# Optimization experiments

Hardware: AMD Instinct MI355X
Metric: run time of the kernel (lower is better)

The kernel has to match this reference:

```python
import jax, jax.numpy as jnp
import numpy as np

N_USERS, N_ITEMS = 100000, 100000
N_NODES = N_USERS + N_ITEMS
N_EDGES = 4000000
USER_DIM, ITEM_DIM = 256, 128
COMMON, HIDDEN, OUT = 64, 64, 32


def setup_inputs() -> dict:
    key = jax.random.key(0)
    ks = jax.random.split(key, 12)
    inp = {
        "user_tensor": jax.random.normal(ks[0], (N_USERS, USER_DIM), jnp.float32),
        "item_tensor": jax.random.normal(ks[1], (N_ITEMS, ITEM_DIM), jnp.float32),
        "edge_index": jax.random.randint(ks[2], (2, N_EDGES), 0, N_NODES, jnp.int64),
        "edge_weight": jax.random.uniform(ks[3], (N_EDGES,), jnp.float32),
        # user_proj / item_proj (nn.Linear: y = x @ W + b)
        "Wu": jax.random.normal(ks[4], (USER_DIM, COMMON), jnp.float32) / np.sqrt(USER_DIM),
        "bu": jnp.zeros((COMMON,), jnp.float32),
        "Wi": jax.random.normal(ks[5], (ITEM_DIM, COMMON), jnp.float32) / np.sqrt(ITEM_DIM),
        "bi": jnp.zeros((COMMON,), jnp.float32),
        # GCNConv layers (linear without bias + separate bias)
        "W1": jax.random.normal(ks[6], (COMMON, HIDDEN), jnp.float32) / np.sqrt(COMMON),
        "b1": jnp.zeros((HIDDEN,), jnp.float32),
        "W2": jax.random.normal(ks[7], (HIDDEN, OUT), jnp.float32) / np.sqrt(HIDDEN),
        "b2": jnp.zeros((OUT,), jnp.float32),
    }
    return inp


def gcn_conv(x, W, b, src, dst, ew, num_nodes):
    """PyG GCNConv: add self-loops (weight 1), symmetric deg norm, transform, scatter-add."""
    x = x @ W  # transform first: [N, out]
    loop = jnp.arange(num_nodes, dtype=src.dtype)
    src2 = jnp.concatenate([src, loop])
    dst2 = jnp.concatenate([dst, loop])
    ew2 = jnp.concatenate([ew, jnp.ones((num_nodes,), x.dtype)])
    deg = jax.ops.segment_sum(ew2, dst2, num_segments=num_nodes)
    dinv = jnp.where(deg > 0, jax.lax.rsqrt(deg), 0.0)
    norm = dinv[src2] * ew2 * dinv[dst2]  # [E+N]
    msgs = x[src2] * norm[:, None]  # gather + scale: [E+N, out]
    return jax.ops.segment_sum(msgs, dst2, num_segments=num_nodes) + b


def reference(user_tensor, item_tensor, edge_index, edge_weight,
              Wu, bu, Wi, bi, W1, b1, W2, b2):
    user_emb = user_tensor @ Wu + bu
    item_emb = item_tensor @ Wi + bi
    x = jnp.concatenate([user_emb, item_emb], axis=0)  # [N_NODES, COMMON]
    src, dst = edge_index[0], edge_index[1]
    x = gcn_conv(x, W1, b1, src, dst, edge_weight, N_NODES)
    x = jax.nn.relu(x)
    x = gcn_conv(x, W2, b2, src, dst, edge_weight, N_NODES)
    return x
```

## Files before the change

kernel.cpp:

```cpp
#include <hip/hip_runtime.h>
#include <hip/hip_bf16.h>

#define N_USERS_C 100000
#define N_ITEMS_C 100000
#define N_NODES_C 200000
#define USER_DIM_C 256
#define ITEM_DIM_C 128
#define COMMON_C 64
#define HIDDEN_C 64
#define OUT_DIM_C 32

#define CB_BITS 8
#define CB_NODES 256
#define NCB ((N_NODES_C + CB_NODES - 1) / CB_NODES)
#define CB_CAP 5632
#define B_THREADS 256
#define B_UNROLL (CB_CAP / B_THREADS)

#define BIN_GRID 512
#define BIN_CHUNK_MAX 8192
#define MAX_EPT 8

#define UBLK 1563

typedef unsigned int uint32;
typedef __bf16 bf16x8 __attribute__((ext_vector_type(8)));
typedef float f32x4 __attribute__((ext_vector_type(4)));



__device__ __forceinline__ float bf2f(ushort u) { return __uint_as_float(((unsigned)u) << 16); }
__device__ __forceinline__ ushort f2bf(float f) {
    unsigned u = __float_as_uint(f);
    return (ushort)((u + 0x7FFFu + ((u >> 16) & 1u)) >> 16);
}
__device__ __forceinline__ void store4(float* p, float a, float b, float c, float d) {
    *(float4*)p = make_float4(a, b, c, d);
}
__device__ __forceinline__ void store4(ushort* p, float a, float b, float c, float d) {
    ushort4 u;
    u.x = f2bf(a); u.y = f2bf(b); u.z = f2bf(c); u.w = f2bf(d);
    *(ushort4*)p = u;
}

union ABFrag {
    uint4 q;
    ushort u[8];
    bf16x8 v;
};


__device__ __forceinline__ void wt_one(const float* W, ushort* WT, int K, int N, int i) {
    int k = i / N, n = i % N;
    WT[(size_t)n * K + k] = f2bf(W[i]);
}


__global__ __launch_bounds__(1024) void bin_kernel(
        const int* __restrict__ src, const int* __restrict__ dst,
        const float* __restrict__ ew, int* __restrict__ bucket_cnt,
        uint2* __restrict__ rec2, int E, int chunk,
        const float* __restrict__ Wu, const float* __restrict__ Wi,
        const float* __restrict__ W1, const float* __restrict__ W2,
        ushort* __restrict__ wtU, ushort* __restrict__ wtI,
        ushort* __restrict__ wt1, ushort* __restrict__ wt2) {
    {
        const int SU = USER_DIM_C * 64, SI = ITEM_DIM_C * 64, S1 = 64 * 64, S2 = 64 * 32;
        int i = blockIdx.x * 1024 + threadIdx.x;
        if (i < SU + SI + S1 + S2) {
            if (i < SU) wt_one(Wu, wtU, USER_DIM_C, 64, i);
            else if ((i -= SU) < SI) wt_one(Wi, wtI, ITEM_DIM_C, 64, i);
            else if ((i -= SI) < S1) wt_one(W1, wt1, 64, 64, i);
            else wt_one(W2, wt2, 64, 32, i - S1);
        }
    }

    __shared__ int hist[NCB];
    __shared__ int cur[NCB];
    for (int i = threadIdx.x; i < NCB; i += 1024) hist[i] = 0;
    __syncthreads();
    const int beg = blockIdx.x * chunk;
    const int end = min(E, beg + chunk);

    int dc[MAX_EPT];
#pragma unroll
    for (int s = 0; s < MAX_EPT / 4; ++s) {
        const int e0 = beg + (threadIdx.x << 2) + (s << 12);
        int4 d4 = make_int4(-1, -1, -1, -1);
        if (e0 + 3 < end) {
            d4 = *(const int4*)(dst + e0);
        } else if (e0 < end) {
            d4.x = dst[e0];
            if (e0 + 1 < end) d4.y = dst[e0 + 1];
            if (e0 + 2 < end) d4.z = dst[e0 + 2];
        }
        dc[s * 4 + 0] = d4.x; dc[s * 4 + 1] = d4.y;
        dc[s * 4 + 2] = d4.z; dc[s * 4 + 3] = d4.w;
        if (d4.x >= 0) atomicAdd(&hist[d4.x >> CB_BITS], 1);
        if (d4.y >= 0) atomicAdd(&hist[d4.y >> CB_BITS], 1);
        if (d4.z >= 0) atomicAdd(&hist[d4.z >> CB_BITS], 1);
        if (d4.w >= 0) atomicAdd(&hist[d4.w >> CB_BITS], 1);
    }
    __syncthreads();

    for (int i = threadIdx.x; i < NCB; i += 1024) {
        const int h = hist[i];
        cur[i] = h ? atomicAdd(&bucket_cnt[i], h) : 0;
    }
    __syncthreads();

#pragma unroll
    for (int s = 0; s < MAX_EPT / 4; ++s) {
        const int e0 = beg + (threadIdx.x << 2) + (s << 12);
        if (e0 >= end) continue;
        int4 s4;
        float4 w4;
        if (e0 + 3 < end) {
            s4 = *(const int4*)(src + e0);
            w4 = *(const float4*)(ew + e0);
        } else {
            s4 = make_int4(0, 0, 0, 0);
            w4 = make_float4(0, 0, 0, 0);
            s4.x = src[e0]; w4.x = ew[e0];
            if (e0 + 1 < end) { s4.y = src[e0 + 1]; w4.y = ew[e0 + 1]; }
            if (e0 + 2 < end) { s4.z = src[e0 + 2]; w4.z = ew[e0 + 2]; }
        }
        const int dv[4] = {dc[s * 4 + 0], dc[s * 4 + 1], dc[s * 4 + 2], dc[s * 4 + 3]};
        const int sv[4] = {s4.x, s4.y, s4.z, s4.w};
        const float wv[4] = {w4.x, w4.y, w4.z, w4.w};
#pragma unroll
        for (int k = 0; k < 4; ++k) {
            const int d = dv[k];
            if (d < 0) continue;
            uint32 q = (uint32)(wv[k] * 255.0f + 0.5f);
            if (q > 255u) q = 255u;
            const int b = d >> CB_BITS;
            const int slot = atomicAdd(&cur[b], 1);
            if (slot < CB_CAP)
                rec2[(size_t)b * CB_CAP + slot] =
                    make_uint2((((uint32)sv[k]) << 8) | q, (uint32)d);
        }
    }
}


__global__ __launch_bounds__(B_THREADS) void region_build_kernel(
        const uint2* __restrict__ rec2, const int* __restrict__ bucket_cnt,
        uint32* __restrict__ csr32, int* __restrict__ row_beg,
        int* __restrict__ row_cnt, float* __restrict__ dinv) {
    __shared__ int pk[CB_NODES];
    __shared__ int s[CB_NODES];
    __shared__ int cur[CB_NODES];
    const int cb = blockIdx.x;
    const int node0 = cb << CB_BITS;
    int total = bucket_cnt[cb];
    if (total > CB_CAP) total = CB_CAP;
    const uint2* r = rec2 + (size_t)cb * CB_CAP;

    pk[threadIdx.x] = 0;
    __syncthreads();

    uint2 rr[B_UNROLL];
#pragma unroll
    for (int u = 0; u < B_UNROLL; ++u) {
        const int j = threadIdx.x + u * B_THREADS;
        if (j < total) {
            rr[u] = r[j];
            atomicAdd(&pk[rr[u].y & (CB_NODES - 1)],
                      (int)((1u << 20) | (rr[u].x & 255u)));
        } else {
            rr[u] = make_uint2(0u, 0xFFFFFFFFu);
        }
    }
    __syncthreads();

    const int v = pk[threadIdx.x] >> 20;
    s[threadIdx.x] = v;
    __syncthreads();
#pragma unroll
    for (int off = 1; off < CB_NODES; off <<= 1) {
        const int t = (threadIdx.x >= off) ? s[threadIdx.x - off] : 0;
        __syncthreads();
        s[threadIdx.x] += t;
        __syncthreads();
    }
    {
        const int ex = s[threadIdx.x] - v;
        const int node = node0 + threadIdx.x;
        const int abs0 = cb * (2 * CB_CAP) + ex;
        if (node < N_NODES_C) {
            row_beg[node] = abs0;
            row_cnt[node] = v;
            dinv[node] = rsqrtf(1.0f + (float)(pk[threadIdx.x] & 0xFFFFF) * (1.0f / 255.0f));
        }
        cur[threadIdx.x] = abs0;
    }
    __syncthreads();

#pragma unroll
    for (int u = 0; u < B_UNROLL; ++u) {
        if (rr[u].y != 0xFFFFFFFFu) {
            const int slot = atomicAdd(&cur[rr[u].y & (CB_NODES - 1)], 1);
            csr32[slot] = rr[u].x;
        }
    }
}


template <int K>
__global__ __launch_bounds__(256) void fused_proj_kernel(
        const float* __restrict__ X, const ushort* __restrict__ WT,
        const ushort* __restrict__ wt1, const float* __restrict__ bias,
        const float* __restrict__ dinv, ushort* __restrict__ y1, int node0) {
    __shared__ ushort elds[64][72];
    const int lane = threadIdx.x & 63;
    const int wave = threadIdx.x >> 6;
    const int lr = lane & 15;
    const int quad = lane >> 4;

    const int M = N_USERS_C;
    const int m0 = blockIdx.x * 64 + wave * 16;

    f32x4 acc[4];
#pragma unroll
    for (int nt = 0; nt < 4; ++nt) acc[nt] = (f32x4){0.0f, 0.0f, 0.0f, 0.0f};

    int arow = m0 + lr;
    if (arow >= M) arow = M - 1;
    const float* Xr = X + (size_t)arow * K;

#pragma unroll
    for (int kc = 0; kc < K; kc += 32) {
        const int k0 = kc + quad * 8;
        float4 x0 = *(const float4*)(Xr + k0);
        float4 x1 = *(const float4*)(Xr + k0 + 4);
        ABFrag a;
        a.u[0] = f2bf(x0.x); a.u[1] = f2bf(x0.y); a.u[2] = f2bf(x0.z); a.u[3] = f2bf(x0.w);
        a.u[4] = f2bf(x1.x); a.u[5] = f2bf(x1.y); a.u[6] = f2bf(x1.z); a.u[7] = f2bf(x1.w);
#pragma unroll
        for (int nt = 0; nt < 4; ++nt) {
            ABFrag bf;
            bf.q = *(const uint4*)(WT + (size_t)(nt * 16 + lr) * K + k0);
            acc[nt] = __builtin_amdgcn_mfma_f32_16x16x32_bf16(a.v, bf.v, acc[nt], 0, 0, 0);
        }
    }

#pragma unroll
    for (int r = 0; r < 4; ++r) {
        const int row_l = wave * 16 + quad * 4 + r;
#pragma unroll
        for (int nt = 0; nt < 4; ++nt) {
            const int n = nt * 16 + lr;
            elds[row_l][n] = f2bf(acc[nt][r] + bias[n]);
        }
    }
    __syncthreads();

    f32x4 acc2[4];
#pragma unroll
    for (int nt = 0; nt < 4; ++nt) acc2[nt] = (f32x4){0.0f, 0.0f, 0.0f, 0.0f};

#pragma unroll
    for (int kc = 0; kc < 64; kc += 32) {
        const int k0 = kc + quad * 8;
        ABFrag a;
        a.q = *(const uint4*)(&elds[wave * 16 + lr][k0]);
#pragma unroll
        for (int nt = 0; nt < 4; ++nt) {
            ABFrag bf;
            bf.q = *(const uint4*)(wt1 + (size_t)(nt * 16 + lr) * 64 + k0);
            acc2[nt] = __builtin_amdgcn_mfma_f32_16x16x32_bf16(a.v, bf.v, acc2[nt], 0, 0, 0);
        }
    }

#pragma unroll
    for (int r = 0; r < 4; ++r) {
        const int m = m0 + quad * 4 + r;
        if (m < M) {
            const int node = node0 + m;
            const float sc = dinv[node];
#pragma unroll
            for (int nt = 0; nt < 4; ++nt) {
                y1[(size_t)node * 64 + nt * 16 + lr] = f2bf(acc2[nt][r] * sc);
            }
        }
    }
}

template <int K, int NT, bool XF32, bool SCALE>
__global__ __launch_bounds__(256) void mfma_proj_kernel(const void* __restrict__ Xv,
                                                        const ushort* __restrict__ WT,
                                                        const float* __restrict__ bias,
                                                        const float* __restrict__ dinvp,
                                                        ushort* __restrict__ Y, int M) {
    const int lane = threadIdx.x & 63;
    const int wave = threadIdx.x >> 6;
    const int lr = lane & 15;
    const int quad = lane >> 4;
    const int m0 = blockIdx.x * 64 + wave * 16;
    const int N = NT * 16;

    f32x4 acc[NT];
#pragma unroll
    for (int nt = 0; nt < NT; ++nt) acc[nt] = (f32x4){0.0f, 0.0f, 0.0f, 0.0f};

    int arow = m0 + lr;
    if (arow >= M) arow = M - 1;
    const size_t abase = (size_t)arow * K;

#pragma unroll
    for (int kc = 0; kc < K; kc += 32) {
        const int k0 = kc + quad * 8;
        ABFrag a;
        if (XF32) {
            const float* Xf = (const float*)Xv;
            float4 x0 = *(const float4*)(Xf + abase + k0);
            float4 x1 = *(const float4*)(Xf + abase + k0 + 4);
            a.u[0] = f2bf(x0.x); a.u[1] = f2bf(x0.y); a.u[2] = f2bf(x0.z); a.u[3] = f2bf(x0.w);
            a.u[4] = f2bf(x1.x); a.u[5] = f2bf(x1.y); a.u[6] = f2bf(x1.z); a.u[7] = f2bf(x1.w);
        } else {
            const ushort* Xb = (const ushort*)Xv;
            a.q = *(const uint4*)(Xb + abase + k0);
        }
#pragma unroll
        for (int nt = 0; nt < NT; ++nt) {
            ABFrag bf;
            bf.q = *(const uint4*)(WT + (size_t)(nt * 16 + lr) * K + k0);
            acc[nt] = __builtin_amdgcn_mfma_f32_16x16x32_bf16(a.v, bf.v, acc[nt], 0, 0, 0);
        }
    }

#pragma unroll
    for (int r = 0; r < 4; ++r) {
        const int m = m0 + quad * 4 + r;
        if (m < M) {
            const float sc = SCALE ? dinvp[m] : 1.0f;
#pragma unroll
            for (int nt = 0; nt < NT; ++nt) {
                const int n = nt * 16 + lr;
                const float bc = bias ? bias[n] : 0.0f;
                Y[(size_t)m * N + n] = f2bf((acc[nt][r] + bc) * sc);
            }
        }
    }
}


template <int N, bool RELU, typename TY>
__global__ void gather_kernel(const int* __restrict__ row_beg, const int* __restrict__ row_cnt,
                              const uint32* __restrict__ csr, const ushort* __restrict__ y,
                              const float* __restrict__ dinv, const float* __restrict__ b,
                              TY* __restrict__ out) {
    constexpr int LPN = N / 4;
    const int node = blockIdx.x * (256 / LPN) + threadIdx.x / LPN;
    const int c0 = (threadIdx.x % LPN) * 4;

    const int beg = row_beg[node];
    const int end = beg + row_cnt[node];

    float a0[4] = {0, 0, 0, 0}, a1[4] = {0, 0, 0, 0}, a2[4] = {0, 0, 0, 0}, a3[4] = {0, 0, 0, 0};
    int j = beg;
    for (; j + 4 <= end; j += 4) {
        uint32 e0 = csr[j], e1 = csr[j + 1], e2 = csr[j + 2], e3 = csr[j + 3];
        int s0 = e0 >> 8, s1 = e1 >> 8, s2 = e2 >> 8, s3 = e3 >> 8;
        float c0v = (float)(e0 & 255u) * (1.0f / 255.0f);
        float c1v = (float)(e1 & 255u) * (1.0f / 255.0f);
        float c2v = (float)(e2 & 255u) * (1.0f / 255.0f);
        float c3v = (float)(e3 & 255u) * (1.0f / 255.0f);
        ushort4 u0 = *(const ushort4*)(y + (size_t)s0 * N + c0);
        ushort4 u1 = *(const ushort4*)(y + (size_t)s1 * N + c0);
        ushort4 u2 = *(const ushort4*)(y + (size_t)s2 * N + c0);
        ushort4 u3 = *(const ushort4*)(y + (size_t)s3 * N + c0);
        a0[0] += bf2f(u0.x) * c0v; a0[1] += bf2f(u0.y) * c0v;
        a0[2] += bf2f(u0.z) * c0v; a0[3] += bf2f(u0.w) * c0v;
        a1[0] += bf2f(u1.x) * c1v; a1[1] += bf2f(u1.y) * c1v;
        a1[2] += bf2f(u1.z) * c1v; a1[3] += bf2f(u1.w) * c1v;
        a2[0] += bf2f(u2.x) * c2v; a2[1] += bf2f(u2.y) * c2v;
        a2[2] += bf2f(u2.z) * c2v; a2[3] += bf2f(u2.w) * c2v;
        a3[0] += bf2f(u3.x) * c3v; a3[1] += bf2f(u3.y) * c3v;
        a3[2] += bf2f(u3.z) * c3v; a3[3] += bf2f(u3.w) * c3v;
    }
    for (; j < end; ++j) {
        uint32 e = csr[j];
        int s = e >> 8;
        float cv = (float)(e & 255u) * (1.0f / 255.0f);
        ushort4 u = *(const ushort4*)(y + (size_t)s * N + c0);
        a0[0] += bf2f(u.x) * cv; a0[1] += bf2f(u.y) * cv;
        a0[2] += bf2f(u.z) * cv; a0[3] += bf2f(u.w) * cv;
    }
    const float di = dinv[node];
    ushort4 us = *(const ushort4*)(y + (size_t)node * N + c0);
    float4 bc = *(const float4*)(b + c0);
    float r0 = (((a0[0] + a1[0]) + (a2[0] + a3[0])) + bf2f(us.x)) * di + bc.x;
    float r1 = (((a0[1] + a1[1]) + (a2[1] + a3[1])) + bf2f(us.y)) * di + bc.y;
    float r2 = (((a0[2] + a1[2]) + (a2[2] + a3[2])) + bf2f(us.z)) * di + bc.z;
    float r3 = (((a0[3] + a1[3]) + (a2[3] + a3[3])) + bf2f(us.w)) * di + bc.w;
    if (RELU) {
        r0 = fmaxf(r0, 0.0f); r1 = fmaxf(r1, 0.0f);
        r2 = fmaxf(r2, 0.0f); r3 = fmaxf(r3, 0.0f);
    }
    store4(&out[(size_t)node * N + c0], r0, r1, r2, r3);
}


extern "C" void kernel_launch(void* const* d_in, const int* in_sizes, int n_in,
                              void* d_out, int out_size, void* d_ws, size_t ws_size,
                              hipStream_t stream) {
    const float* user = (const float*)d_in[0];
    const float* item = (const float*)d_in[1];
    const int* ei = (const int*)d_in[2];
    const float* ew = (const float*)d_in[3];
    const float* Wu = (const float*)d_in[4];
    const float* bu = (const float*)d_in[5];
    const float* Wi = (const float*)d_in[6];
    const float* bi = (const float*)d_in[7];
    const float* W1 = (const float*)d_in[8];
    const float* b1 = (const float*)d_in[9];
    const float* W2 = (const float*)d_in[10];
    const float* b2 = (const float*)d_in[11];
    float* out = (float*)d_out;

    const int E = in_sizes[3];
    const int* src = ei;
    const int* dst = ei + E;
    const int NB = N_NODES_C;
    const int nblk = (E > BIN_GRID * BIN_CHUNK_MAX) ? ((E + BIN_CHUNK_MAX - 1) / BIN_CHUNK_MAX)
                                                    : BIN_GRID;
    const int chunk = (((E + nblk - 1) / nblk) + 3) & ~3;

    char* p = (char*)d_ws;
    uint2* rec2 = (uint2*)p;   p += (size_t)NCB * CB_CAP * 8;
    ushort* y1 = (ushort*)p;   p += (size_t)NB * 64 * 2;
    ushort* h1 = (ushort*)p;   p += (size_t)NB * 64 * 2;
    ushort* y2 = (ushort*)p;   p += (size_t)NB * 32 * 2;
    int* bucket_cnt = (int*)p; p += (size_t)NCB * 4;
    int* row_beg = (int*)p;    p += (size_t)NB * 4;
    int* row_cnt = (int*)p;    p += (size_t)NB * 4;
    float* dinv = (float*)p;   p += (size_t)NB * 4;
    ushort* wtU = (ushort*)p;  p += (size_t)USER_DIM_C * 64 * 2;
    ushort* wtI = (ushort*)p;  p += (size_t)ITEM_DIM_C * 64 * 2;
    ushort* wt1 = (ushort*)p;  p += (size_t)64 * 64 * 2;
    ushort* wt2 = (ushort*)p;  p += (size_t)64 * 32 * 2;

    uint32* csr = (uint32*)rec2;

    hipMemsetAsync(bucket_cnt, 0, (size_t)NCB * 4, stream);
    bin_kernel<<<nblk, 1024, 0, stream>>>(src, dst, ew, bucket_cnt, rec2, E, chunk,
                                          Wu, Wi, W1, W2, wtU, wtI, wt1, wt2);
    region_build_kernel<<<NCB, B_THREADS, 0, stream>>>(rec2, bucket_cnt, csr, row_beg, row_cnt,
                                                       dinv);

    fused_proj_kernel<USER_DIM_C><<<UBLK, 256, 0, stream>>>(user, wtU, wt1, bu, dinv, y1, 0);
    fused_proj_kernel<ITEM_DIM_C><<<UBLK, 256, 0, stream>>>(item, wtI, wt1, bi, dinv, y1,
                                                            N_USERS_C);

    gather_kernel<64, true><<<NB / 16, 256, 0, stream>>>(row_beg, row_cnt, csr, y1, dinv, b1, h1);

    mfma_proj_kernel<64, 2, false, true><<<NB / 64, 256, 0, stream>>>(
        h1, wt2, (const float*)nullptr, dinv, y2, NB);
    gather_kernel<32, false><<<NB / 32, 256, 0, stream>>>(row_beg, row_cnt, csr, y2, dinv, b2, out);
}
```

Measured before the change: 509.8 us.

## Fuse layer-1 gather with layer-2 projection and merge user/item projection launches

Merges the user and item projection kernels into one launch that dispatches by block index, and hoists all input loads ahead of the MFMA loop so more memory requests are in flight. Fuses the first GCN aggregation (with bias and ReLU) with the second linear transform: each block stages 16 aggregated rows in shared memory and one wave runs the 64x32 MFMA, so the h1 intermediate is never written to or read back from global memory. This removes one kernel launch and a full intermediate round trip. In exchange, only one wave per block does the MFMA step and the hoisted loads raise register use.

```diff
diff --git a/kernel.cpp b/kernel.cpp
--- a/kernel.cpp
+++ b/kernel.cpp
@@ -36,11 +36,6 @@
 }
 __device__ __forceinline__ void store4(float* p, float a, float b, float c, float d) {
     *(float4*)p = make_float4(a, b, c, d);
-}
-__device__ __forceinline__ void store4(ushort* p, float a, float b, float c, float d) {
-    ushort4 u;
-    u.x = f2bf(a); u.y = f2bf(b); u.z = f2bf(c); u.w = f2bf(d);
-    *(ushort4*)p = u;
 }
 
 union ABFrag {
@@ -208,40 +203,51 @@
 
 
 template <int K>
-__global__ __launch_bounds__(256) void fused_proj_kernel(
+__device__ __forceinline__ void fused_proj_body(
         const float* __restrict__ X, const ushort* __restrict__ WT,
         const ushort* __restrict__ wt1, const float* __restrict__ bias,
-        const float* __restrict__ dinv, ushort* __restrict__ y1, int node0) {
-    __shared__ ushort elds[64][72];
+        const float* __restrict__ dinv, ushort* __restrict__ y1, int node0, int mb,
+        ushort (*elds)[72]) {
+    constexpr int NK = K / 32;
     const int lane = threadIdx.x & 63;
     const int wave = threadIdx.x >> 6;
     const int lr = lane & 15;
     const int quad = lane >> 4;
 
     const int M = N_USERS_C;
-    const int m0 = blockIdx.x * 64 + wave * 16;
-
-    f32x4 acc[4];
-#pragma unroll
-    for (int nt = 0; nt < 4; ++nt) acc[nt] = (f32x4){0.0f, 0.0f, 0.0f, 0.0f};
+    const int m0 = mb * 64 + wave * 16;
 
     int arow = m0 + lr;
     if (arow >= M) arow = M - 1;
-    const float* Xr = X + (size_t)arow * K;
-
-#pragma unroll
-    for (int kc = 0; kc < K; kc += 32) {
-        const int k0 = kc + quad * 8;
-        float4 x0 = *(const float4*)(Xr + k0);
-        float4 x1 = *(const float4*)(Xr + k0 + 4);
-        ABFrag a;
-        a.u[0] = f2bf(x0.x); a.u[1] = f2bf(x0.y); a.u[2] = f2bf(x0.z); a.u[3] = f2bf(x0.w);
-        a.u[4] = f2bf(x1.x); a.u[5] = f2bf(x1.y); a.u[6] = f2bf(x1.z); a.u[7] = f2bf(x1.w);
+    const float* Xr = X + (size_t)arow * K + quad * 8;
+
+    float4 xf[2 * NK];
+#pragma unroll
+    for (int t = 0; t < NK; ++t) {
+        xf[2 * t] = *(const float4*)(Xr + t * 32);
+        xf[2 * t + 1] = *(const float4*)(Xr + t * 32 + 4);
+    }
+    ABFrag xa[NK];
+#pragma unroll
+    for (int t = 0; t < NK; ++t) {
+        xa[t].u[0] = f2bf(xf[2 * t].x); xa[t].u[1] = f2bf(xf[2 * t].y);
+        xa[t].u[2] = f2bf(xf[2 * t].z); xa[t].u[3] = f2bf(xf[2 * t].w);
+        xa[t].u[4] = f2bf(xf[2 * t + 1].x); xa[t].u[5] = f2bf(xf[2 * t + 1].y);
+        xa[t].u[6] = f2bf(xf[2 * t + 1].z); xa[t].u[7] = f2bf(xf[2 * t + 1].w);
+    }
+
+    f32x4 acc[4];
+#pragma unroll
+    for (int nt = 0; nt < 4; ++nt) acc[nt] = (f32x4){0.0f, 0.0f, 0.0f, 0.0f};
+
+#pragma unroll
+    for (int t = 0; t < NK; ++t) {
+        const int k0 = t * 32 + quad * 8;
 #pragma unroll
         for (int nt = 0; nt < 4; ++nt) {
             ABFrag bf;
             bf.q = *(const uint4*)(WT + (size_t)(nt * 16 + lr) * K + k0);
-            acc[nt] = __builtin_amdgcn_mfma_f32_16x16x32_bf16(a.v, bf.v, acc[nt], 0, 0, 0);
+            acc[nt] = __builtin_amdgcn_mfma_f32_16x16x32_bf16(xa[t].v, bf.v, acc[nt], 0, 0, 0);
         }
     }
 
@@ -287,59 +293,104 @@
     }
 }
 
-template <int K, int NT, bool XF32, bool SCALE>
-__global__ __launch_bounds__(256) void mfma_proj_kernel(const void* __restrict__ Xv,
-                                                        const ushort* __restrict__ WT,
-                                                        const float* __restrict__ bias,
-                                                        const float* __restrict__ dinvp,
-                                                        ushort* __restrict__ Y, int M) {
-    const int lane = threadIdx.x & 63;
-    const int wave = threadIdx.x >> 6;
-    const int lr = lane & 15;
-    const int quad = lane >> 4;
-    const int m0 = blockIdx.x * 64 + wave * 16;
-    const int N = NT * 16;
-
-    f32x4 acc[NT];
-#pragma unroll
-    for (int nt = 0; nt < NT; ++nt) acc[nt] = (f32x4){0.0f, 0.0f, 0.0f, 0.0f};
-
-    int arow = m0 + lr;
-    if (arow >= M) arow = M - 1;
-    const size_t abase = (size_t)arow * K;
-
-#pragma unroll
-    for (int kc = 0; kc < K; kc += 32) {
-        const int k0 = kc + quad * 8;
-        ABFrag a;
-        if (XF32) {
-            const float* Xf = (const float*)Xv;
-            float4 x0 = *(const float4*)(Xf + abase + k0);
-            float4 x1 = *(const float4*)(Xf + abase + k0 + 4);
-            a.u[0] = f2bf(x0.x); a.u[1] = f2bf(x0.y); a.u[2] = f2bf(x0.z); a.u[3] = f2bf(x0.w);
-            a.u[4] = f2bf(x1.x); a.u[5] = f2bf(x1.y); a.u[6] = f2bf(x1.z); a.u[7] = f2bf(x1.w);
-        } else {
-            const ushort* Xb = (const ushort*)Xv;
-            a.q = *(const uint4*)(Xb + abase + k0);
-        }
-#pragma unroll
-        for (int nt = 0; nt < NT; ++nt) {
-            ABFrag bf;
-            bf.q = *(const uint4*)(WT + (size_t)(nt * 16 + lr) * K + k0);
-            acc[nt] = __builtin_amdgcn_mfma_f32_16x16x32_bf16(a.v, bf.v, acc[nt], 0, 0, 0);
-        }
-    }
-
-#pragma unroll
-    for (int r = 0; r < 4; ++r) {
-        const int m = m0 + quad * 4 + r;
-        if (m < M) {
-            const float sc = SCALE ? dinvp[m] : 1.0f;
-#pragma unroll
-            for (int nt = 0; nt < NT; ++nt) {
-                const int n = nt * 16 + lr;
-                const float bc = bias ? bias[n] : 0.0f;
-                Y[(size_t)m * N + n] = f2bf((acc[nt][r] + bc) * sc);
+__global__ __launch_bounds__(256) void fused_proj_kernel(
+        const float* __restrict__ user, const float* __restrict__ item,
+        const ushort* __restrict__ wtU, const ushort* __restrict__ wtI,
+        const ushort* __restrict__ wt1, const float* __restrict__ bu,
+        const float* __restrict__ bi, const float* __restrict__ dinv,
+        ushort* __restrict__ y1) {
+    __shared__ ushort elds[64][72];
+    if (blockIdx.x < UBLK)
+        fused_proj_body<USER_DIM_C>(user, wtU, wt1, bu, dinv, y1, 0, blockIdx.x, elds);
+    else
+        fused_proj_body<ITEM_DIM_C>(item, wtI, wt1, bi, dinv, y1, N_USERS_C,
+                                    blockIdx.x - UBLK, elds);
+}
+
+
+__global__ __launch_bounds__(256) void gather_mm_kernel(
+        const int* __restrict__ row_beg, const int* __restrict__ row_cnt,
+        const uint32* __restrict__ csr, const ushort* __restrict__ y,
+        const float* __restrict__ dinv, const float* __restrict__ b,
+        const ushort* __restrict__ wt2, ushort* __restrict__ y2) {
+    __shared__ ushort hlds[16][72];
+    const int g = threadIdx.x >> 4;
+    const int c0 = (threadIdx.x & 15) * 4;
+    const int node = blockIdx.x * 16 + g;
+
+    const int beg = row_beg[node];
+    const int end = beg + row_cnt[node];
+
+    float a0[4] = {0, 0, 0, 0}, a1[4] = {0, 0, 0, 0}, a2[4] = {0, 0, 0, 0}, a3[4] = {0, 0, 0, 0};
+    int j = beg;
+    for (; j + 4 <= end; j += 4) {
+        uint32 e0 = csr[j], e1 = csr[j + 1], e2 = csr[j + 2], e3 = csr[j + 3];
+        int s0 = e0 >> 8, s1 = e1 >> 8, s2 = e2 >> 8, s3 = e3 >> 8;
+        float c0v = (float)(e0 & 255u) * (1.0f / 255.0f);
+        float c1v = (float)(e1 & 255u) * (1.0f / 255.0f);
+        float c2v = (float)(e2 & 255u) * (1.0f / 255.0f);
+        float c3v = (float)(e3 & 255u) * (1.0f / 255.0f);
+        ushort4 u0 = *(const ushort4*)(y + (size_t)s0 * 64 + c0);
+        ushort4 u1 = *(const ushort4*)(y + (size_t)s1 * 64 + c0);
+        ushort4 u2 = *(const ushort4*)(y + (size_t)s2 * 64 + c0);
+        ushort4 u3 = *(const ushort4*)(y + (size_t)s3 * 64 + c0);
+        a0[0] += bf2f(u0.x) * c0v; a0[1] += bf2f(u0.y) * c0v;
+        a0[2] += bf2f(u0.z) * c0v; a0[3] += bf2f(u0.w) * c0v;
+        a1[0] += bf2f(u1.x) * c1v; a1[1] += bf2f(u1.y) * c1v;
+        a1[2] += bf2f(u1.z) * c1v; a1[3] += bf2f(u1.w) * c1v;
+        a2[0] += bf2f(u2.x) * c2v; a2[1] += bf2f(u2.y) * c2v;
+        a2[2] += bf2f(u2.z) * c2v; a2[3] += bf2f(u2.w) * c2v;
+        a3[0] += bf2f(u3.x) * c3v; a3[1] += bf2f(u3.y) * c3v;
+        a3[2] += bf2f(u3.z) * c3v; a3[3] += bf2f(u3.w) * c3v;
+    }
+    for (; j < end; ++j) {
+        uint32 e = csr[j];
+        int s = e >> 8;
+        float cv = (float)(e & 255u) * (1.0f / 255.0f);
+        ushort4 u = *(const ushort4*)(y + (size_t)s * 64 + c0);
+        a0[0] += bf2f(u.x) * cv; a0[1] += bf2f(u.y) * cv;
+        a0[2] += bf2f(u.z) * cv; a0[3] += bf2f(u.w) * cv;
+    }
+    const float di = dinv[node];
+    ushort4 us = *(const ushort4*)(y + (size_t)node * 64 + c0);
+    float4 bc = *(const float4*)(b + c0);
+    float r0 = (((a0[0] + a1[0]) + (a2[0] + a3[0])) + bf2f(us.x)) * di + bc.x;
+    float r1 = (((a0[1] + a1[1]) + (a2[1] + a3[1])) + bf2f(us.y)) * di + bc.y;
+    float r2 = (((a0[2] + a1[2]) + (a2[2] + a3[2])) + bf2f(us.z)) * di + bc.z;
+    float r3 = (((a0[3] + a1[3]) + (a2[3] + a3[3])) + bf2f(us.w)) * di + bc.w;
+    r0 = fmaxf(r0, 0.0f); r1 = fmaxf(r1, 0.0f);
+    r2 = fmaxf(r2, 0.0f); r3 = fmaxf(r3, 0.0f);
+
+    ushort4 hu;
+    hu.x = f2bf(r0); hu.y = f2bf(r1); hu.z = f2bf(r2); hu.w = f2bf(r3);
+    *(ushort4*)&hlds[g][c0] = hu;
+    __syncthreads();
+
+    if (threadIdx.x < 64) {
+        const int lr = threadIdx.x & 15;
+        const int quad = threadIdx.x >> 4;
+        f32x4 acc[2];
+        acc[0] = (f32x4){0.0f, 0.0f, 0.0f, 0.0f};
+        acc[1] = (f32x4){0.0f, 0.0f, 0.0f, 0.0f};
+#pragma unroll
+        for (int kc = 0; kc < 64; kc += 32) {
+            const int k0 = kc + quad * 8;
+            ABFrag a;
+            a.q = *(const uint4*)(&hlds[lr][k0]);
+#pragma unroll
+            for (int nt = 0; nt < 2; ++nt) {
+                ABFrag bf;
+                bf.q = *(const uint4*)(wt2 + (size_t)(nt * 16 + lr) * 64 + k0);
+                acc[nt] = __builtin_amdgcn_mfma_f32_16x16x32_bf16(a.v, bf.v, acc[nt], 0, 0, 0);
+            }
+        }
+#pragma unroll
+        for (int r = 0; r < 4; ++r) {
+            const int nd = blockIdx.x * 16 + quad * 4 + r;
+            const float sc = dinv[nd];
+#pragma unroll
+            for (int nt = 0; nt < 2; ++nt) {
+                y2[(size_t)nd * 32 + nt * 16 + lr] = f2bf(acc[nt][r] * sc);
             }
         }
     }
@@ -431,7 +482,6 @@
     char* p = (char*)d_ws;
     uint2* rec2 = (uint2*)p;   p += (size_t)NCB * CB_CAP * 8;
     ushort* y1 = (ushort*)p;   p += (size_t)NB * 64 * 2;
-    ushort* h1 = (ushort*)p;   p += (size_t)NB * 64 * 2;
     ushort* y2 = (ushort*)p;   p += (size_t)NB * 32 * 2;
     int* bucket_cnt = (int*)p; p += (size_t)NCB * 4;
     int* row_beg = (int*)p;    p += (size_t)NB * 4;
@@ -450,13 +500,9 @@
     region_build_kernel<<<NCB, B_THREADS, 0, stream>>>(rec2, bucket_cnt, csr, row_beg, row_cnt,
                                                        dinv);
 
-    fused_proj_kernel<USER_DIM_C><<<UBLK, 256, 0, stream>>>(user, wtU, wt1, bu, dinv, y1, 0);
-    fused_proj_kernel<ITEM_DIM_C><<<UBLK, 256, 0, stream>>>(item, wtI, wt1, bi, dinv, y1,
-                                                            N_USERS_C);
-
-    gather_kernel<64, true><<<NB / 16, 256, 0, stream>>>(row_beg, row_cnt, csr, y1, dinv, b1, h1);
-
-    mfma_proj_kernel<64, 2, false, true><<<NB / 64, 256, 0, stream>>>(
-        h1, wt2, (const float*)nullptr, dinv, y2, NB);
+    fused_proj_kernel<<<2 * UBLK, 256, 0, stream>>>(user, item, wtU, wtI, wt1, bu, bi, dinv, y1);
+
+    gather_mm_kernel<<<NB / 16, 256, 0, stream>>>(row_beg, row_cnt, csr, y1, dinv, b1, wt2, y2);
+
     gather_kernel<32, false><<<NB / 32, 256, 0, stream>>>(row_beg, row_cnt, csr, y2, dinv, b2, out);
 }
```

Result: faster. 486.9 us (-4.5%).
